# Performance work log

Measured on AMD Instinct MI355X. Metric: run time of the kernel, lower is better.

## Reference

```python
import jax, jax.numpy as jnp
import numpy as np
from jax import lax

B, C_IN, C_OUT, H, W = 2, 128, 256, 128, 128
KH = KW = 3
K = KH * KW  # 9 kernel sampling locations
EPS = 1e-5


def setup_inputs() -> dict:
    ks = jax.random.split(jax.random.key(0), 9)
    x = jax.random.normal(ks[0], (B, C_IN, H, W), dtype=jnp.float32)
    # offset/mask conv: 27 = 3*K output channels, 3x3 kernel, stride 1, same pad
    w_off = jax.random.normal(ks[1], (3 * K, C_IN, KH, KW), dtype=jnp.float32) * 0.01
    b_off = jnp.zeros((3 * K,), dtype=jnp.float32)
    # deformable conv weight [C_out, C_in, 3, 3] + bias
    w_dcn = jax.random.normal(ks[2], (C_OUT, C_IN, KH, KW), dtype=jnp.float32) * (1.0 / np.sqrt(C_IN * K))
    b_dcn = jax.random.normal(ks[3], (C_OUT,), dtype=jnp.float32) * 0.01
    # BatchNorm (inference-mode) params
    gamma = 1.0 + 0.1 * jax.random.normal(ks[4], (C_OUT,), dtype=jnp.float32)
    beta = 0.1 * jax.random.normal(ks[5], (C_OUT,), dtype=jnp.float32)
    moving_mean = 0.1 * jax.random.normal(ks[6], (C_OUT,), dtype=jnp.float32)
    moving_var = jax.random.uniform(ks[7], (C_OUT,), dtype=jnp.float32, minval=0.5, maxval=1.5)
    return {"x": x, "w_off": w_off, "b_off": b_off, "w_dcn": w_dcn, "b_dcn": b_dcn,
            "gamma": gamma, "beta": beta, "moving_mean": moving_mean, "moving_var": moving_var}


def _conv2d_nchw(x, w, b):
    y = lax.conv_general_dilated(x, w, window_strides=(1, 1), padding='SAME',
                                 dimension_numbers=('NCHW', 'OIHW', 'NCHW'))
    return y + b[None, :, None, None]


def _bilinear_gather(x, yi, xi):
    """Gather x[b,:,yi,xi] with zero padding outside. x:[B,C,H,W]; yi,xi:[B,K,H,W] int."""
    valid = ((yi >= 0) & (yi < H) & (xi >= 0) & (xi < W)).astype(x.dtype)  # [B,K,H,W]
    yc = jnp.clip(yi, 0, H - 1)
    xc = jnp.clip(xi, 0, W - 1)
    idx = (yc * W + xc).reshape(B, -1)  # [B, K*H*W]
    xf = x.reshape(B, C_IN, H * W)
    g = jax.vmap(lambda xb, ib: xb[:, ib])(xf, idx)  # [B, C, K*H*W]
    return g.reshape(B, C_IN, K, H, W) * valid[:, None]


def _deform_conv(x, offset, mask, w, b):
    """DCNv2 modulated deformable conv, 3x3, stride 1, SAME (pad=1).
    offset: [B, 2K, H, W] with (dy, dx) interleaved per kernel location (tfa/DCNv2 layout).
    mask:   [B, K, H, W] (already sigmoided).
    """
    dy = offset[:, 0::2]  # [B,K,H,W]
    dx = offset[:, 1::2]
    ky = (jnp.arange(K, dtype=jnp.float32) // KW) - 1.0  # kernel y offsets in {-1,0,1}
    kx = (jnp.arange(K, dtype=jnp.float32) % KW) - 1.0
    ii = jnp.arange(H, dtype=jnp.float32)[:, None]
    jj = jnp.arange(W, dtype=jnp.float32)[None, :]
    py = ii[None, None] + ky[None, :, None, None] + dy  # [B,K,H,W] sampling y
    px = jj[None, None] + kx[None, :, None, None] + dx  # [B,K,H,W] sampling x

    y0f = jnp.floor(py)
    x0f = jnp.floor(px)
    wy = (py - y0f)[:, None]  # [B,1,K,H,W]
    wx = (px - x0f)[:, None]
    y0 = y0f.astype(jnp.int32)
    x0 = x0f.astype(jnp.int32)

    v00 = _bilinear_gather(x, y0, x0)
    v01 = _bilinear_gather(x, y0, x0 + 1)
    v10 = _bilinear_gather(x, y0 + 1, x0)
    v11 = _bilinear_gather(x, y0 + 1, x0 + 1)
    val = (v00 * (1 - wy) * (1 - wx) + v01 * (1 - wy) * wx
           + v10 * wy * (1 - wx) + v11 * wy * wx)  # [B,C,K,H,W]
    val = val * mask[:, None]  # modulation

    w_r = w.reshape(C_OUT, C_IN, K)
    out = jnp.einsum('bckhw,ock->bohw', val, w_r)
    return out + b[None, :, None, None]


def reference(x, w_off, b_off, w_dcn, b_dcn, gamma, beta, moving_mean, moving_var):
    weight_info = _conv2d_nchw(x, w_off, b_off)  # [B, 27, H, W]
    o1, o2, m = jnp.split(weight_info, 3, axis=1)
    offset = jnp.concatenate((o1, o2), axis=1)  # [B, 18, H, W]
    mask = jax.nn.sigmoid(m)  # [B, 9, H, W]
    y = _deform_conv(x, offset, mask, w_dcn, b_dcn)
    # BatchNorm2d (inference, channels_first) + ReLU
    inv = gamma / jnp.sqrt(moving_var + EPS)
    y = (y - moving_mean[None, :, None, None]) * inv[None, :, None, None] + beta[None, :, None, None]
    return jax.nn.relu(y)
```

## Files before the change

kernel.cpp:

```cpp
#include <hip/hip_runtime.h>
#include <hip/hip_fp16.h>

#define HH 128
#define WW 128
#define CIN 128
#define COUT 256
#define K9 9
#define HW (HH*WW)
#define PIX (2*HW)
#define KDIM (CIN*K9)
#define BN_EPS 1e-5f

typedef __attribute__((ext_vector_type(8))) short short8;
typedef __attribute__((ext_vector_type(4))) float f32x4;
typedef _Float16 half8 __attribute__((ext_vector_type(8)));
typedef unsigned short u16;
typedef unsigned int u32;

union H8 { short8 s; __half2 h2[4]; half8 h; };

struct __align__(16) Meta16 { ushort4 idx; __half2 w01, w23; };
static_assert(sizeof(Meta16) == 16, "");

__device__ __forceinline__ u16 f2h(float f) {
    union { __half h; u16 u; } x; x.h = __float2half_rn(f); return x.u;
}

__global__ __launch_bounds__(256) void prep_all(
    const float* __restrict__ x, const float* __restrict__ w_dcn,
    const float* __restrict__ w_off, u16* __restrict__ xt,
    u16* __restrict__ wT2, u16* __restrict__ wOffT2)
{
    __shared__ float tile[32][129];
    if (blockIdx.x < 1024) {
        const int b   = blockIdx.x >> 9;
        const int hw0 = (blockIdx.x & 511) * 32;
        const float* __restrict__ xb = x + (size_t)b * (CIN*HW);
        #pragma unroll
        for (int i = 0; i < 16; ++i) {
            const int idx = threadIdx.x + i*256;
            const int c = idx >> 5, hwl = idx & 31;
            tile[hwl][c] = xb[(size_t)c*HW + hw0 + hwl];
        }
        __syncthreads();
        const int hwl = threadIdx.x >> 3;
        const int c0  = (threadIdx.x & 7) * 16;
        short8 s0, s1;
        #pragma unroll
        for (int j = 0; j < 8; ++j) {
            s0[j] = (short)f2h(tile[hwl][c0 + j]);
            s1[j] = (short)f2h(tile[hwl][c0 + 8 + j]);
        }
        u16* dst = xt + ((size_t)b*HW + hw0 + hwl)*CIN + c0;
        *(short8*)dst = s0;
        *(short8*)(dst + 8) = s1;
    } else {
        const int u2 = (blockIdx.x - 1024) * 2 + (threadIdx.x >> 7);
        const int c  = threadIdx.x & 127;
        const int k  = u2 % 9;
        const int o  = u2 / 9;
        const int s = c >> 5, ch = c & 31;
        const int tt = k*4 + s;
        if (o < COUT) {
            wT2[((size_t)tt*COUT + o)*32 + ch] =
                f2h(w_dcn[(size_t)o*KDIM + c*K9 + k]);
        } else {
            const int j = o - COUT;
            wOffT2[((size_t)tt*32 + j)*32 + ch] =
                (j < 27) ? f2h(w_off[(size_t)j*KDIM + c*K9 + k]) : (u16)0;
        }
    }
}

__global__ __launch_bounds__(512, 4) __attribute__((amdgpu_waves_per_eu(4, 4)))
void dcn_fused(
    const u16* __restrict__ xt, const u16* __restrict__ wT2,
    const u16* __restrict__ wOffT2, const float* __restrict__ b_off,
    const float* __restrict__ b_dcn, const float* __restrict__ gamma,
    const float* __restrict__ beta, const float* __restrict__ mmean,
    const float* __restrict__ mvar, float* __restrict__ out)
{
    __shared__ __align__(16) u16 Vs[2][64*128];
    __shared__ __align__(16) Meta16 metaL[K9*64];

    const int t = threadIdx.x, l = t & 63, wv = t >> 6;
    const int l15 = l & 15, lq = l >> 4;
    const int bid = (blockIdx.x & 7) * 64 + (blockIdx.x >> 3);
    const int pg0 = bid * 64;
    const int b   = pg0 >> 14;
    const int hw0 = pg0 & 16383;
    const u16* __restrict__ xtb = xt + (size_t)b * (HW*CIN);

    {
        const int pxg = wv & 3;
        const int ks  = wv >> 2;
        const int px  = pxg*16 + l15;
        const int pg  = pg0 + px;
        const int hw  = pg & 16383;
        const int h = hw >> 7, w = hw & 127;
        f32x4 oa0 = {0.f,0.f,0.f,0.f}, oa1 = {0.f,0.f,0.f,0.f};
        #pragma unroll
        for (int it = 0; it < 18; ++it) {
            const int tt = ks*18 + it;
            const int k = tt >> 2, c0 = (tt & 3) * 32;
            const int yy = h + (k/3) - 1, xx = w + (k%3) - 1;
            const bool valid = ((unsigned)yy < HH) && ((unsigned)xx < WW);
            const int idx = min(max(yy,0),HH-1)*WW + min(max(xx,0),WW-1);
            H8 bv, a0, a1;
            bv.s = *(const short8*)(xtb + (size_t)idx*CIN + c0 + lq*8);
            a0.s = *(const short8*)(wOffT2 + ((size_t)tt*32 + l15)*32      + lq*8);
            a1.s = *(const short8*)(wOffT2 + ((size_t)tt*32 + 16 + l15)*32 + lq*8);
            if (!valid) bv.s = (short8){0,0,0,0,0,0,0,0};
            oa0 = __builtin_amdgcn_mfma_f32_16x16x32_f16(a0.h, bv.h, oa0, 0,0,0);
            oa1 = __builtin_amdgcn_mfma_f32_16x16x32_f16(a1.h, bv.h, oa1, 0,0,0);
        }
        float* plane = (float*)&Vs[ks][0];
        #pragma unroll
        for (int r = 0; r < 4; ++r) {
            plane[px*33 + lq*4 + r]      = oa0[r];
            plane[px*33 + 16 + lq*4 + r] = oa1[r];
        }
        __syncthreads();

        const float* __restrict__ p0 = (const float*)&Vs[0][0];
        const float* __restrict__ p1 = (const float*)&Vs[1][0];
        #pragma unroll
        for (int rd = 0; rd < 2; ++rd) {
            const int u = t + rd*512;
            if (u < 576) {
                const int px2 = u & 63, k = u >> 6;
                const int hwp = (pg0 + px2) & 16383;
                const int hp = hwp >> 7, wp = hwp & 127;
                const float dy = p0[px2*33 + 2*k]     + p1[px2*33 + 2*k]     + b_off[2*k];
                const float dx = p0[px2*33 + 2*k + 1] + p1[px2*33 + 2*k + 1] + b_off[2*k+1];
                const float mm = p0[px2*33 + 18 + k]  + p1[px2*33 + 18 + k]  + b_off[18+k];
                const float py = (float)hp + (float)(k/3) - 1.0f + dy;
                const float px_ = (float)wp + (float)(k%3) - 1.0f + dx;
                const float msk = 1.0f / (1.0f + expf(-mm));
                const float y0f = floorf(py), x0f = floorf(px_);
                const float wy = py - y0f, wx = px_ - x0f;
                const int y0 = (int)y0f, x0 = (int)x0f;
                const int y1 = y0 + 1,   x1 = x0 + 1;
                const bool v00 = ((unsigned)y0 < HH) && ((unsigned)x0 < WW);
                const bool v01 = ((unsigned)y0 < HH) && ((unsigned)x1 < WW);
                const bool v10 = ((unsigned)y1 < HH) && ((unsigned)x0 < WW);
                const bool v11 = ((unsigned)y1 < HH) && ((unsigned)x1 < WW);
                const int y0c = min(max(y0,0),HH-1), y1c = min(max(y1,0),HH-1);
                const int x0c = min(max(x0,0),WW-1), x1c = min(max(x1,0),WW-1);
                Meta16 mo;
                mo.idx.x = (u16)(y0c*WW + x0c);
                mo.idx.y = (u16)(y0c*WW + x1c);
                mo.idx.z = (u16)(y1c*WW + x0c);
                mo.idx.w = (u16)(y1c*WW + x1c);
                const float f00 = v00 ? (1.f-wy)*(1.f-wx)*msk : 0.f;
                const float f01 = v01 ? (1.f-wy)*wx*msk       : 0.f;
                const float f10 = v10 ? wy*(1.f-wx)*msk       : 0.f;
                const float f11 = v11 ? wy*wx*msk             : 0.f;
                mo.w01 = __floats2half2_rn(f00, f01);
                mo.w23 = __floats2half2_rn(f10, f11);
                metaL[k*64 + px2] = mo;
            }
        }
        __syncthreads();
    }

    const int pxl  = t >> 3;
    const int cb   = t & 7;
    const int px15 = pxl & 15;

    f32x4 acc[8];
    #pragma unroll
    for (int i = 0; i < 8; ++i) acc[i] = (f32x4){0.f,0.f,0.f,0.f};

    const u16 *g0, *g1, *g2, *g3;
    __half2 wb0, wb1, wb2, wb3;

#define SETMETA(k_) do { \
    const Meta16 mt_ = metaL[(k_)*64 + pxl]; \
    g0 = xtb + (size_t)mt_.idx.x*CIN + cb*8; \
    g1 = xtb + (size_t)mt_.idx.y*CIN + cb*8; \
    g2 = xtb + (size_t)mt_.idx.z*CIN + cb*8; \
    g3 = xtb + (size_t)mt_.idx.w*CIN + cb*8; \
    wb0 = __half2half2(__low2half(mt_.w01)); \
    wb1 = __half2half2(__high2half(mt_.w01)); \
    wb2 = __half2half2(__low2half(mt_.w23)); \
    wb3 = __half2half2(__high2half(mt_.w23)); \
} while (0)

#define ISSUE(cr_, u_) do { \
    cr_[0].s = *(const short8*)(g0 + (u_)*64); \
    cr_[1].s = *(const short8*)(g1 + (u_)*64); \
    cr_[2].s = *(const short8*)(g2 + (u_)*64); \
    cr_[3].s = *(const short8*)(g3 + (u_)*64); \
} while (0)

#define COMBINE_WRITE(cr_, u_, buf_) do { \
    H8 r_; \
    _Pragma("unroll") \
    for (int i_ = 0; i_ < 4; ++i_) \
        r_.h2[i_] = __hfma2(cr_[3].h2[i_], wb3, __hfma2(cr_[2].h2[i_], wb2, \
                    __hfma2(cr_[1].h2[i_], wb1, __hmul2(cr_[0].h2[i_], wb0)))); \
    *(short8*)&Vs[buf_][pxl*128 + ((cb + (u_)*8) ^ px15)*8] = r_.s; \
} while (0)

    H8 cA[4], cB[4];
    SETMETA(0);
    ISSUE(cA, 0); ISSUE(cB, 1);
    COMBINE_WRITE(cA, 0, 0); COMBINE_WRITE(cB, 1, 0);
    __syncthreads();

    int cur = 0;
    for (int k = 0; k < 9; ++k) {
        const bool pf = (k < 8);
        H8 av[4][2];
        #pragma unroll
        for (int s = 0; s < 4; ++s)
            #pragma unroll
            for (int m = 0; m < 2; ++m)
                av[s][m].s = *(const short8*)
                    (wT2 + ((size_t)(k*4 + s)*COUT + wv*32 + m*16 + l15)*32 + lq*8);
        __builtin_amdgcn_sched_barrier(0);
        if (pf) { SETMETA(k+1); ISSUE(cA, 0); ISSUE(cB, 1); }
        __builtin_amdgcn_sched_barrier(0);

        #pragma unroll
        for (int s = 0; s < 4; ++s) {
            #pragma unroll
            for (int nh = 0; nh < 2; ++nh) {
                H8 bf[2];
                #pragma unroll
                for (int j = 0; j < 2; ++j) {
                    const int n = nh*2 + j;
                    bf[j].s = *(const short8*)
                        &Vs[cur][(n*16 + l15)*128 + ((s*4 + lq) ^ l15)*8];
                }
                #pragma unroll
                for (int m = 0; m < 2; ++m)
                    #pragma unroll
                    for (int j = 0; j < 2; ++j)
                        acc[m*4 + nh*2 + j] =
                            __builtin_amdgcn_mfma_f32_16x16x32_f16(
                                av[s][m].h, bf[j].h, acc[m*4 + nh*2 + j], 0, 0, 0);
            }
        }
        if (pf) { COMBINE_WRITE(cA, 0, cur ^ 1); COMBINE_WRITE(cB, 1, cur ^ 1); }
        __syncthreads();
        cur ^= 1;
    }
#undef SETMETA
#undef ISSUE
#undef COMBINE_WRITE

    #pragma unroll
    for (int m = 0; m < 2; ++m) {
        #pragma unroll
        for (int r = 0; r < 4; ++r) {
            const int o = wv*32 + m*16 + lq*4 + r;
            const float sc = gamma[o] * rsqrtf(mvar[o] + BN_EPS);
            const float sh = (b_dcn[o] - mmean[o]) * sc + beta[o];
            float* __restrict__ op = out + ((size_t)(b*COUT + o) << 14) + hw0;
            #pragma unroll
            for (int n = 0; n < 4; ++n) {
                const float v = fmaf(acc[m*4 + n][r], sc, sh);
                op[n*16 + l15] = fmaxf(v, 0.f);
            }
        }
    }
}

extern "C" void kernel_launch(void* const* d_in, const int* in_sizes, int n_in,
                              void* d_out, int out_size, void* d_ws, size_t ws_size,
                              hipStream_t stream) {
    (void)in_sizes; (void)n_in; (void)out_size; (void)ws_size;
    const float* x      = (const float*)d_in[0];
    const float* w_off  = (const float*)d_in[1];
    const float* b_off  = (const float*)d_in[2];
    const float* w_dcn  = (const float*)d_in[3];
    const float* b_dcn  = (const float*)d_in[4];
    const float* gamma  = (const float*)d_in[5];
    const float* beta   = (const float*)d_in[6];
    const float* mmean  = (const float*)d_in[7];
    const float* mvar   = (const float*)d_in[8];
    float* out = (float*)d_out;

    char* ws = (char*)d_ws;
    u16* xtp    = (u16*)ws;
    u16* wT2    = (u16*)(ws + 8388608);
    u16* wOffT2 = (u16*)(ws + 8388608 + 589824);

    prep_all <<<dim3(1024 + 1296), 256, 0, stream>>>(x, w_dcn, w_off,
                                                     xtp, wT2, wOffT2);
    dcn_fused<<<dim3(PIX/64), 512, 0, stream>>>(xtp, wT2, wOffT2, b_off, b_dcn,
                                                gamma, beta, mmean, mvar, out);
}
```

Baseline: 64.04 us.

## Stage a 7-row input window in LDS and loop over channel groups

The deformable gather now first copies a 7-row window of the transposed fp16 input (per 32-channel group) into shared memory. Bilinear samples that fall inside the window are read from LDS, and out-of-window samples fall back to global loads. The weight layout changes to channel-group-major, and the main loop becomes cg×k with only 256 threads doing the combine. This aims to cut scattered global gather traffic, at the cost of more barriers, per-group window reloads, and half the threads idle during the combine.

```diff
diff --git a/kernel.cpp b/kernel.cpp
--- a/kernel.cpp
+++ b/kernel.cpp
@@ -10,6 +10,7 @@
 #define PIX (2*HW)
 #define KDIM (CIN*K9)
 #define BN_EPS 1e-5f
+#define WROWS 7
 
 typedef __attribute__((ext_vector_type(8))) short short8;
 typedef __attribute__((ext_vector_type(4))) float f32x4;
@@ -25,11 +26,12 @@
 __device__ __forceinline__ u16 f2h(float f) {
     union { __half h; u16 u; } x; x.h = __float2half_rn(f); return x.u;
 }
+__device__ __forceinline__ int swz(int px) { return (px & 3) ^ ((px >> 2) & 3); }
 
 __global__ __launch_bounds__(256) void prep_all(
     const float* __restrict__ x, const float* __restrict__ w_dcn,
     const float* __restrict__ w_off, u16* __restrict__ xt,
-    u16* __restrict__ wT2, u16* __restrict__ wOffT2)
+    u16* __restrict__ wT3, u16* __restrict__ wOffT3)
 {
     __shared__ float tile[32][129];
     if (blockIdx.x < 1024) {
@@ -59,14 +61,14 @@
         const int c  = threadIdx.x & 127;
         const int k  = u2 % 9;
         const int o  = u2 / 9;
-        const int s = c >> 5, ch = c & 31;
-        const int tt = k*4 + s;
+        const int q  = (c >> 5)*9 + k;
+        const int ch = c & 31;
         if (o < COUT) {
-            wT2[((size_t)tt*COUT + o)*32 + ch] =
+            wT3[((size_t)q*COUT + o)*32 + ch] =
                 f2h(w_dcn[(size_t)o*KDIM + c*K9 + k]);
         } else {
             const int j = o - COUT;
-            wOffT2[((size_t)tt*32 + j)*32 + ch] =
+            wOffT3[((size_t)q*32 + j)*32 + ch] =
                 (j < 27) ? f2h(w_off[(size_t)j*KDIM + c*K9 + k]) : (u16)0;
         }
     }
@@ -74,13 +76,14 @@
 
 __global__ __launch_bounds__(512, 4) __attribute__((amdgpu_waves_per_eu(4, 4)))
 void dcn_fused(
-    const u16* __restrict__ xt, const u16* __restrict__ wT2,
-    const u16* __restrict__ wOffT2, const float* __restrict__ b_off,
+    const u16* __restrict__ xt, const u16* __restrict__ wT3,
+    const u16* __restrict__ wOffT3, const float* __restrict__ b_off,
     const float* __restrict__ b_dcn, const float* __restrict__ gamma,
     const float* __restrict__ beta, const float* __restrict__ mmean,
     const float* __restrict__ mvar, float* __restrict__ out)
 {
-    __shared__ __align__(16) u16 Vs[2][64*128];
+    __shared__ __align__(16) u16 win[WROWS*128*4*8];
+    __shared__ __align__(16) u16 Vs[2][64*4*8];
     __shared__ __align__(16) Meta16 metaL[K9*64];
 
     const int t = threadIdx.x, l = t & 63, wv = t >> 6;
@@ -89,32 +92,35 @@
     const int pg0 = bid * 64;
     const int b   = pg0 >> 14;
     const int hw0 = pg0 & 16383;
+    const int hrow = hw0 >> 7;
+    const int wlo  = min(max(hrow - 3, 0), HH - WROWS);
     const u16* __restrict__ xtb = xt + (size_t)b * (HW*CIN);
 
     {
         const int pxg = wv & 3;
         const int ks  = wv >> 2;
         const int px  = pxg*16 + l15;
-        const int pg  = pg0 + px;
-        const int hw  = pg & 16383;
+        const int hw  = (pg0 + px) & 16383;
         const int h = hw >> 7, w = hw & 127;
         f32x4 oa0 = {0.f,0.f,0.f,0.f}, oa1 = {0.f,0.f,0.f,0.f};
         #pragma unroll
         for (int it = 0; it < 18; ++it) {
-            const int tt = ks*18 + it;
-            const int k = tt >> 2, c0 = (tt & 3) * 32;
+            const int q  = ks*18 + it;
+            const int cg = 2*ks + (it / 9);
+            const int k  = it % 9;
+            const int c0 = cg * 32;
             const int yy = h + (k/3) - 1, xx = w + (k%3) - 1;
             const bool valid = ((unsigned)yy < HH) && ((unsigned)xx < WW);
             const int idx = min(max(yy,0),HH-1)*WW + min(max(xx,0),WW-1);
             H8 bv, a0, a1;
             bv.s = *(const short8*)(xtb + (size_t)idx*CIN + c0 + lq*8);
-            a0.s = *(const short8*)(wOffT2 + ((size_t)tt*32 + l15)*32      + lq*8);
-            a1.s = *(const short8*)(wOffT2 + ((size_t)tt*32 + 16 + l15)*32 + lq*8);
+            a0.s = *(const short8*)(wOffT3 + ((size_t)q*32 + l15)*32      + lq*8);
+            a1.s = *(const short8*)(wOffT3 + ((size_t)q*32 + 16 + l15)*32 + lq*8);
             if (!valid) bv.s = (short8){0,0,0,0,0,0,0,0};
             oa0 = __builtin_amdgcn_mfma_f32_16x16x32_f16(a0.h, bv.h, oa0, 0,0,0);
             oa1 = __builtin_amdgcn_mfma_f32_16x16x32_f16(a1.h, bv.h, oa1, 0,0,0);
         }
-        float* plane = (float*)&Vs[ks][0];
+        float* plane = (float*)win + ks * (64*33);
         #pragma unroll
         for (int r = 0; r < 4; ++r) {
             plane[px*33 + lq*4 + r]      = oa0[r];
@@ -122,8 +128,8 @@
         }
         __syncthreads();
 
-        const float* __restrict__ p0 = (const float*)&Vs[0][0];
-        const float* __restrict__ p1 = (const float*)&Vs[1][0];
+        const float* __restrict__ p0 = (const float*)win;
+        const float* __restrict__ p1 = (const float*)win + 64*33;
         #pragma unroll
         for (int rd = 0; rd < 2; ++rd) {
             const int u = t + rd*512;
@@ -164,92 +170,90 @@
         __syncthreads();
     }
 
-    const int pxl  = t >> 3;
-    const int cb   = t & 7;
-    const int px15 = pxl & 15;
+    const int pxs = t >> 2;
+    const int chl = t & 3;
 
     f32x4 acc[8];
     #pragma unroll
     for (int i = 0; i < 8; ++i) acc[i] = (f32x4){0.f,0.f,0.f,0.f};
 
-    const u16 *g0, *g1, *g2, *g3;
-    __half2 wb0, wb1, wb2, wb3;
-
-#define SETMETA(k_) do { \
-    const Meta16 mt_ = metaL[(k_)*64 + pxl]; \
-    g0 = xtb + (size_t)mt_.idx.x*CIN + cb*8; \
-    g1 = xtb + (size_t)mt_.idx.y*CIN + cb*8; \
-    g2 = xtb + (size_t)mt_.idx.z*CIN + cb*8; \
-    g3 = xtb + (size_t)mt_.idx.w*CIN + cb*8; \
-    wb0 = __half2half2(__low2half(mt_.w01)); \
-    wb1 = __half2half2(__high2half(mt_.w01)); \
-    wb2 = __half2half2(__low2half(mt_.w23)); \
-    wb3 = __half2half2(__high2half(mt_.w23)); \
+#define WLD(dst_, i_) \
+    dst_.s = *(const short8*)(xtb + (size_t)((wlo + (i_))*WW + pxs)*CIN \
+                              + cg*32 + chl*8)
+#define WWR(i_, v_) \
+    *(short8*)&win[(((i_)*128 + pxs)*4 + (chl ^ swz(pxs)))*8] = v_.s
+
+#define COMBINE(k_, buf_) do { \
+    if (t < 256) { \
+        const Meta16 mt_ = metaL[(k_)*64 + pxs]; \
+        const __half2 wb0_ = __half2half2(__low2half(mt_.w01)); \
+        const __half2 wb1_ = __half2half2(__high2half(mt_.w01)); \
+        const __half2 wb2_ = __half2half2(__low2half(mt_.w23)); \
+        const __half2 wb3_ = __half2half2(__high2half(mt_.w23)); \
+        H8 c_[4]; \
+        const int hwv_[4] = { mt_.idx.x, mt_.idx.y, mt_.idx.z, mt_.idx.w }; \
+        _Pragma("unroll") \
+        for (int j_ = 0; j_ < 4; ++j_) { \
+            const int y_ = hwv_[j_] >> 7, x_ = hwv_[j_] & 127; \
+            const int yr_ = y_ - wlo; \
+            if ((unsigned)yr_ < (unsigned)WROWS) { \
+                c_[j_].s = *(const short8*)&win[((yr_*128 + x_)*4 \
+                                                + (chl ^ swz(x_)))*8]; \
+            } else { \
+                c_[j_].s = *(const short8*)(xtb + (size_t)hwv_[j_]*CIN \
+                                            + cg*32 + chl*8); \
+            } \
+        } \
+        H8 r_; \
+        _Pragma("unroll") \
+        for (int i_ = 0; i_ < 4; ++i_) \
+            r_.h2[i_] = __hfma2(c_[3].h2[i_], wb3_, \
+                        __hfma2(c_[2].h2[i_], wb2_, \
+                        __hfma2(c_[1].h2[i_], wb1_, \
+                        __hmul2(c_[0].h2[i_], wb0_)))); \
+        *(short8*)&Vs[buf_][(pxs*4 + (chl ^ swz(pxs)))*8] = r_.s; \
+    } \
 } while (0)
 
-#define ISSUE(cr_, u_) do { \
-    cr_[0].s = *(const short8*)(g0 + (u_)*64); \
-    cr_[1].s = *(const short8*)(g1 + (u_)*64); \
-    cr_[2].s = *(const short8*)(g2 + (u_)*64); \
-    cr_[3].s = *(const short8*)(g3 + (u_)*64); \
-} while (0)
-
-#define COMBINE_WRITE(cr_, u_, buf_) do { \
-    H8 r_; \
-    _Pragma("unroll") \
-    for (int i_ = 0; i_ < 4; ++i_) \
-        r_.h2[i_] = __hfma2(cr_[3].h2[i_], wb3, __hfma2(cr_[2].h2[i_], wb2, \
-                    __hfma2(cr_[1].h2[i_], wb1, __hmul2(cr_[0].h2[i_], wb0)))); \
-    *(short8*)&Vs[buf_][pxl*128 + ((cb + (u_)*8) ^ px15)*8] = r_.s; \
-} while (0)
-
-    H8 cA[4], cB[4];
-    SETMETA(0);
-    ISSUE(cA, 0); ISSUE(cB, 1);
-    COMBINE_WRITE(cA, 0, 0); COMBINE_WRITE(cB, 1, 0);
-    __syncthreads();
-
-    int cur = 0;
-    for (int k = 0; k < 9; ++k) {
-        const bool pf = (k < 8);
-        H8 av[4][2];
-        #pragma unroll
-        for (int s = 0; s < 4; ++s)
+    for (int cg = 0; cg < 4; ++cg) {
+        {
+            H8 s0, s1, s2, s3;
+            WLD(s0, 0); WLD(s1, 1); WLD(s2, 2); WLD(s3, 3);
+            WWR(0, s0); WWR(1, s1); WWR(2, s2); WWR(3, s3);
+            WLD(s0, 4); WLD(s1, 5); WLD(s2, 6);
+            WWR(4, s0); WWR(5, s1); WWR(6, s2);
+        }
+        __syncthreads();
+        COMBINE(0, 0);
+        __syncthreads();
+
+        for (int k = 0; k < 9; ++k) {
+            H8 av[2];
             #pragma unroll
             for (int m = 0; m < 2; ++m)
-                av[s][m].s = *(const short8*)
-                    (wT2 + ((size_t)(k*4 + s)*COUT + wv*32 + m*16 + l15)*32 + lq*8);
-        __builtin_amdgcn_sched_barrier(0);
-        if (pf) { SETMETA(k+1); ISSUE(cA, 0); ISSUE(cB, 1); }
-        __builtin_amdgcn_sched_barrier(0);
-
-        #pragma unroll
-        for (int s = 0; s < 4; ++s) {
-            #pragma unroll
-            for (int nh = 0; nh < 2; ++nh) {
-                H8 bf[2];
+                av[m].s = *(const short8*)
+                    (wT3 + ((size_t)(cg*9 + k)*COUT + wv*32 + m*16 + l15)*32 + lq*8);
+
+            H8 bf[4];
+            #pragma unroll
+            for (int n = 0; n < 4; ++n) {
+                const int px = n*16 + l15;
+                bf[n].s = *(const short8*)&Vs[k & 1][(px*4 + (lq ^ swz(px)))*8];
+            }
+            #pragma unroll
+            for (int m = 0; m < 2; ++m)
                 #pragma unroll
-                for (int j = 0; j < 2; ++j) {
-                    const int n = nh*2 + j;
-                    bf[j].s = *(const short8*)
-                        &Vs[cur][(n*16 + l15)*128 + ((s*4 + lq) ^ l15)*8];
-                }
-                #pragma unroll
-                for (int m = 0; m < 2; ++m)
-                    #pragma unroll
-                    for (int j = 0; j < 2; ++j)
-                        acc[m*4 + nh*2 + j] =
-                            __builtin_amdgcn_mfma_f32_16x16x32_f16(
-                                av[s][m].h, bf[j].h, acc[m*4 + nh*2 + j], 0, 0, 0);
-            }
-        }
-        if (pf) { COMBINE_WRITE(cA, 0, cur ^ 1); COMBINE_WRITE(cB, 1, cur ^ 1); }
-        __syncthreads();
-        cur ^= 1;
-    }
-#undef SETMETA
-#undef ISSUE
-#undef COMBINE_WRITE
+                for (int n = 0; n < 4; ++n)
+                    acc[m*4 + n] = __builtin_amdgcn_mfma_f32_16x16x32_f16(
+                                       av[m].h, bf[n].h, acc[m*4 + n], 0, 0, 0);
+
+            if (k < 8) COMBINE(k + 1, (k + 1) & 1);
+            __syncthreads();
+        }
+    }
+#undef WLD
+#undef WWR
+#undef COMBINE
 
     #pragma unroll
     for (int m = 0; m < 2; ++m) {
@@ -285,11 +289,11 @@
 
     char* ws = (char*)d_ws;
     u16* xtp    = (u16*)ws;
-    u16* wT2    = (u16*)(ws + 8388608);
-    u16* wOffT2 = (u16*)(ws + 8388608 + 589824);
+    u16* wT3    = (u16*)(ws + 8388608);
+    u16* wOffT3 = (u16*)(ws + 8388608 + 589824);
 
     prep_all <<<dim3(1024 + 1296), 256, 0, stream>>>(x, w_dcn, w_off,
-                                                     xtp, wT2, wOffT2);
-    dcn_fused<<<dim3(PIX/64), 512, 0, stream>>>(xtp, wT2, wOffT2, b_off, b_dcn,
+                                                     xtp, wT3, wOffT3);
+    dcn_fused<<<dim3(PIX/64), 512, 0, stream>>>(xtp, wT3, wOffT3, b_off, b_dcn,
                                                 gamma, beta, mmean, mvar, out);
 }
```

After: 72.07 us. +12.5%, slower.
